# Kernel tuning notes

Hardware: AMD Instinct MI355X
Metric: run time of the kernel (lower is better)

## Reference

```python
import jax, jax.numpy as jnp
import numpy as np

BS, T, N = 16, 50, 100
OBS, ACT, HID, LAT = 40, 8, 64, 16
NEG = -9e15


def _gat(x, adj, w, a_src, a_dst, b, concat, alpha=0.2):
    # x: [B, n, fin]; w: [H, fin, fout]
    h = jnp.einsum('bni,hio->bhno', x, w)
    e_src = jnp.einsum('bhno,ho->bhn', h, a_src[..., 0])
    e_dst = jnp.einsum('bhno,ho->bhn', h, a_dst[..., 0])
    e = e_src[:, :, :, None] + e_dst[:, :, None, :]        # [B,H,n,n]
    e = jnp.where(e > 0, e, alpha * e)                     # LeakyReLU
    e = jnp.where(adj[None, None] > 0, e, NEG)             # mask by adjacency
    att = jax.nn.softmax(e, axis=-1)
    hp = jnp.einsum('bhnm,bhmo->bhno', att, h)
    if concat:
        B, H, n, fo = hp.shape
        return jax.nn.elu(hp.transpose(0, 2, 1, 3).reshape(B, n, H * fo) + b)
    return hp.mean(axis=1) + b


def _lstm(x, Wih, Whh, bih, bhh):
    # x: [B, T, H]; PyTorch gate order i, f, g, o
    def step(carry, xt):
        h, c = carry
        g = xt @ Wih + h @ Whh + bih + bhh
        i, f, gg, o = jnp.split(g, 4, axis=-1)
        c = jax.nn.sigmoid(f) * c + jax.nn.sigmoid(i) * jnp.tanh(gg)
        h = jax.nn.sigmoid(o) * jnp.tanh(c)
        return (h, c), h
    h0 = jnp.zeros((x.shape[0], Whh.shape[0]), x.dtype)
    _, ys = jax.lax.scan(step, (h0, h0), x.transpose(1, 0, 2))
    return ys.transpose(1, 0, 2)


def _forward(o, a_prev, m, eps, params, adj):
    (W_obs, b_obs, W_pa, b_pa, W_mk, b_mk, id_emb,
     lWih, lWhh, lbih, lbhh,
     e1w, e1s, e1d, e1b, e2w, e2s, e2d, e2b,
     d1w, d1s, d1d, d1b, d2w, d2s, d2d, d2b,
     d3w, d3s, d3d, d3b) = params
    bs, t, n, _ = o.shape
    # encode: summed embeddings (dropout is identity in eval)
    emb = (o @ W_obs + b_obs) + (a_prev @ W_pa + b_pa) + (m @ W_mk + b_mk) + id_emb[None, None]
    x = emb.transpose(0, 2, 1, 3).reshape(bs * n, t, HID)
    x = _lstm(x, lWih, lWhh, lbih, lbhh)
    x = x.reshape(bs, n, t, HID).transpose(0, 2, 1, 3).reshape(bs * t, n, HID)
    x = _gat(x, adj, e1w, e1s, e1d, e1b, True)
    x = _gat(x, adj, e2w, e2s, e2d, e2b, False)
    logits = x.reshape(bs, t, n, 2 * LAT).mean(axis=-2)    # AverageGlobalPool over nodes
    mu, logvar = jnp.split(logits, 2, axis=-1)
    z = mu + eps * jnp.exp(0.5 * logvar)                   # reparameterize
    zu = jnp.repeat(z[:, :, None, :], n, axis=2)           # RepeatGlobalUnpool
    d = jnp.concatenate([emb, zu], axis=-1).reshape(bs * t, n, HID + LAT)
    d = _gat(d, adj, d1w, d1s, d1d, d1b, True)
    d = _gat(d, adj, d2w, d2s, d2d, d2b, True)
    d = _gat(d, adj, d3w, d3s, d3d, d3b, False)
    a_recon = d.reshape(bs, t, n, ACT) * m
    return a_recon, mu, logvar


def setup_inputs() -> dict:
    key = jax.random.key(0)
    it = iter(jax.random.split(key, 48))
    def nrm(shape, s=0.1):
        return s * jax.random.normal(next(it), shape, jnp.float32)
    inp = {}
    inp['o'] = jax.random.normal(next(it), (BS, T, N, OBS), jnp.float32)
    inp['a_prev'] = jax.random.uniform(next(it), (BS, T, N, ACT), jnp.float32)
    inp['m'] = (jax.random.uniform(next(it), (BS, T, N, ACT)) > 0.5).astype(jnp.float32)
    inp['eps'] = jax.random.normal(next(it), (BS, T, LAT), jnp.float32)
    adj = jax.random.randint(next(it), (N, N), 0, 2).astype(jnp.int32)
    inp['adj'] = adj.at[jnp.arange(N), jnp.arange(N)].set(1)
    inp['W_obs'] = nrm((OBS, HID)); inp['b_obs'] = jnp.zeros((HID,), jnp.float32)
    inp['W_pa'] = nrm((ACT, HID)); inp['b_pa'] = jnp.zeros((HID,), jnp.float32)
    inp['W_mk'] = nrm((ACT, HID)); inp['b_mk'] = jnp.zeros((HID,), jnp.float32)
    inp['id_emb'] = nrm((N, HID), 1.0)
    inp['lWih'] = nrm((HID, 4 * HID)); inp['lWhh'] = nrm((HID, 4 * HID))
    inp['lbih'] = jnp.zeros((4 * HID,), jnp.float32); inp['lbhh'] = jnp.zeros((4 * HID,), jnp.float32)
    def gat_p(pfx, H, fin, fout, bdim):
        inp[pfx + 'w'] = nrm((H, fin, fout))
        inp[pfx + 's'] = nrm((H, fout, 1))
        inp[pfx + 'd'] = nrm((H, fout, 1))
        inp[pfx + 'b'] = jnp.zeros((bdim,), jnp.float32)
    gat_p('e1', 4, HID, HID // 4, HID)
    gat_p('e2', 1, HID, 2 * LAT, 2 * LAT)
    gat_p('d1', 4, LAT + HID, HID // 4, HID)
    gat_p('d2', 4, HID, HID // 4, HID)
    gat_p('d3', 1, HID, ACT, ACT)
    return inp


def reference(o, a_prev, m, eps, adj, W_obs, b_obs, W_pa, b_pa, W_mk, b_mk, id_emb,
              lWih, lWhh, lbih, lbhh,
              e1w, e1s, e1d, e1b, e2w, e2s, e2d, e2b,
              d1w, d1s, d1d, d1b, d2w, d2s, d2d, d2b,
              d3w, d3s, d3d, d3b):
    params = (W_obs, b_obs, W_pa, b_pa, W_mk, b_mk, id_emb,
              lWih, lWhh, lbih, lbhh,
              e1w, e1s, e1d, e1b, e2w, e2s, e2d, e2b,
              d1w, d1s, d1d, d1b, d2w, d2s, d2d, d2b,
              d3w, d3s, d3d, d3b)
    return _forward(o, a_prev, m, eps, params, adj)
```

## Files before the change

kernel.cpp:

```cpp
#include <hip/hip_runtime.h>

#define BS  16
#define TT  50
#define NN  100
#define OBSF 40
#define ACTF 8
#define HIDF 64
#define LATF 16

typedef __attribute__((ext_vector_type(8))) short bf16x8;
typedef __attribute__((ext_vector_type(4))) float f32x4;

__device__ __forceinline__ float sigmf(float x) { return 1.f / (1.f + __expf(-x)); }
__device__ __forceinline__ float tanh_fast(float x) { return 1.f - 2.f / (__expf(2.f * x) + 1.f); }
__device__ __forceinline__ short bf16s_rne(float a) {
    unsigned u = __float_as_uint(a); u += 0x7fffu + ((u >> 16) & 1u);
    return (short)(u >> 16);
}
__device__ __forceinline__ unsigned bf16pk_rne(float a, float b) {
    unsigned ua = __float_as_uint(a); ua += 0x7fffu + ((ua >> 16) & 1u);
    unsigned ub = __float_as_uint(b); ub += 0x7fffu + ((ub >> 16) & 1u);
    return (ua >> 16) | (ub & 0xffff0000u);
}

__global__ void adjmask_kernel(const int* __restrict__ adj, unsigned long long* __restrict__ mask) {
    int n = threadIdx.x;
    if (n < NN) {
        unsigned long long w0 = 0ull, w1 = 0ull;
        for (int m = 0; m < 64; ++m)  if (adj[n * NN + m] > 0) w0 |= (1ull << m);
        for (int m = 64; m < NN; ++m) if (adj[n * NN + m] > 0) w1 |= (1ull << (m - 64));
        mask[2 * n] = w0; mask[2 * n + 1] = w1;
    }
}

__global__ void emb_kernel(const float* __restrict__ o, const float* __restrict__ ap,
                           const float* __restrict__ mk,
                           const float* __restrict__ Wobs, const float* __restrict__ bobs,
                           const float* __restrict__ Wpa, const float* __restrict__ bpa,
                           const float* __restrict__ Wmk, const float* __restrict__ bmk,
                           const float* __restrict__ idemb, float* __restrict__ emb) {
    int g = blockIdx.x;
    int n = g % NN;
    int j = threadIdx.x;
    __shared__ float so[OBSF], sa[ACTF], sm[ACTF];
    if (j < OBSF) so[j] = o[(size_t)g * OBSF + j];
    if (j >= 40 && j < 48) sa[j - 40] = ap[(size_t)g * ACTF + (j - 40)];
    if (j >= 48 && j < 56) sm[j - 48] = mk[(size_t)g * ACTF + (j - 48)];
    __syncthreads();
    float acc = bobs[j] + bpa[j] + bmk[j] + idemb[n * HIDF + j];
    #pragma unroll
    for (int k = 0; k < OBSF; ++k) acc += so[k] * Wobs[k * HIDF + j];
    #pragma unroll
    for (int k = 0; k < ACTF; ++k) acc += sa[k] * Wpa[k * HIDF + j] + sm[k] * Wmk[k * HIDF + j];
    emb[(size_t)g * HIDF + j] = acc;
}

__launch_bounds__(256)
__global__ void lstm_mfma_kernel(const float* __restrict__ emb,
                                 const float* __restrict__ Wih, const float* __restrict__ Whh,
                                 const float* __restrict__ bih, const float* __restrict__ bhh,
                                 float* __restrict__ xenc) {
    constexpr int GSTRIDE = 260;
    __shared__ __align__(16) float gbuf[16 * GSTRIDE];
    __shared__ __align__(16) short embt[2][16 * 72];
    __shared__ __align__(16) short hbuf[16 * 72];

    const int tid = threadIdx.x;
    const int wv = tid >> 6, lane = tid & 63, q = lane >> 4, c = lane & 15;

    const int seq = tid >> 4;
    const int part = tid & 15;
    const int s = blockIdx.x * 16 + seq;
    const int b = s / NN, n = s % NN;
    const size_t ebase = ((size_t)b * (TT * NN) + n) * HIDF + part * 4;
    const int u0 = part * 4;
    const size_t xbase = ((size_t)b * (TT * NN) + n) * HIDF + u0;

    union { short s8[8]; bf16x8 v; } bf[2][2][4];
    {
        const int colb = wv * 64 + c;
        #pragma unroll
        for (int m = 0; m < 2; ++m) {
            const float* W = m ? Whh : Wih;
            #pragma unroll
            for (int kc = 0; kc < 2; ++kc)
                #pragma unroll
                for (int nt = 0; nt < 4; ++nt)
                    #pragma unroll
                    for (int j = 0; j < 8; ++j)
                        bf[m][kc][nt].s8[j] = bf16s_rne(W[(size_t)(kc * 32 + q * 8 + j) * 256 + colb + nt * 16]);
        }
    }
    float4 bi, bfo, bg, bo;
    {
        float* bp[4] = {&bi.x, &bfo.x, &bg.x, &bo.x};
        #pragma unroll
        for (int gsel = 0; gsel < 4; ++gsel)
            #pragma unroll
            for (int r = 0; r < 4; ++r)
                bp[gsel][r] = bih[gsel * 64 + u0 + r] + bhh[gsel * 64 + u0 + r];
    }
    for (int i = tid; i < 16 * 72 / 2; i += 256) ((unsigned*)hbuf)[i] = 0u;
    {
        float4 e0 = *(const float4*)&emb[ebase];
        uint2 pk; pk.x = bf16pk_rne(e0.x, e0.y); pk.y = bf16pk_rne(e0.z, e0.w);
        *(uint2*)&embt[0][seq * 72 + part * 4] = pk;
    }
    float cst[4] = {0.f, 0.f, 0.f, 0.f};
    __syncthreads();

    for (int t = 0; t < TT; ++t) {
        float4 pre;
        if (t + 1 < TT) pre = *(const float4*)&emb[ebase + (size_t)(t + 1) * (NN * HIDF)];
        const short* et = &embt[t & 1][0];
        bf16x8 a_e0 = *(const bf16x8*)&et[c * 72 + q * 8];
        bf16x8 a_e1 = *(const bf16x8*)&et[c * 72 + 32 + q * 8];
        bf16x8 a_h0 = *(const bf16x8*)&hbuf[c * 72 + q * 8];
        bf16x8 a_h1 = *(const bf16x8*)&hbuf[c * 72 + 32 + q * 8];
        f32x4 acc[4];
        #pragma unroll
        for (int nt = 0; nt < 4; ++nt) {
            f32x4 a = {0.f, 0.f, 0.f, 0.f};
            a = __builtin_amdgcn_mfma_f32_16x16x32_bf16(a_e0, bf[0][0][nt].v, a, 0, 0, 0);
            a = __builtin_amdgcn_mfma_f32_16x16x32_bf16(a_e1, bf[0][1][nt].v, a, 0, 0, 0);
            a = __builtin_amdgcn_mfma_f32_16x16x32_bf16(a_h0, bf[1][0][nt].v, a, 0, 0, 0);
            a = __builtin_amdgcn_mfma_f32_16x16x32_bf16(a_h1, bf[1][1][nt].v, a, 0, 0, 0);
            acc[nt] = a;
        }
        #pragma unroll
        for (int nt = 0; nt < 4; ++nt)
            #pragma unroll
            for (int r = 0; r < 4; ++r)
                gbuf[(q * 4 + r) * GSTRIDE + wv * 64 + nt * 16 + c] = acc[nt][r];
        __syncthreads();
        if (t + 1 < TT) {
            uint2 pk; pk.x = bf16pk_rne(pre.x, pre.y); pk.y = bf16pk_rne(pre.z, pre.w);
            *(uint2*)&embt[(t + 1) & 1][seq * 72 + part * 4] = pk;
        }
        float4 gi = *(const float4*)&gbuf[seq * GSTRIDE + u0];
        float4 gf = *(const float4*)&gbuf[seq * GSTRIDE + 64 + u0];
        float4 gg = *(const float4*)&gbuf[seq * GSTRIDE + 128 + u0];
        float4 go = *(const float4*)&gbuf[seq * GSTRIDE + 192 + u0];
        float hv[4];
        {
            float gir[4] = {gi.x + bi.x, gi.y + bi.y, gi.z + bi.z, gi.w + bi.w};
            float gfr[4] = {gf.x + bfo.x, gf.y + bfo.y, gf.z + bfo.z, gf.w + bfo.w};
            float ggr[4] = {gg.x + bg.x, gg.y + bg.y, gg.z + bg.z, gg.w + bg.w};
            float gor[4] = {go.x + bo.x, go.y + bo.y, go.z + bo.z, go.w + bo.w};
            #pragma unroll
            for (int r = 0; r < 4; ++r) {
                cst[r] = sigmf(gfr[r]) * cst[r] + sigmf(gir[r]) * tanh_fast(ggr[r]);
                hv[r] = sigmf(gor[r]) * tanh_fast(cst[r]);
            }
        }
        uint2 hpk; hpk.x = bf16pk_rne(hv[0], hv[1]); hpk.y = bf16pk_rne(hv[2], hv[3]);
        *(uint2*)&hbuf[seq * 72 + u0] = hpk;
        float4 xo; xo.x = hv[0]; xo.y = hv[1]; xo.z = hv[2]; xo.w = hv[3];
        *(float4*)&xenc[xbase + (size_t)t * (NN * HIDF)] = xo;
        __syncthreads();
    }
}

template <int FIN1, int FIN2, int H, int FOUT, int SPLIT, int OUTMODE>
__launch_bounds__(256)
__global__ void gat_kernel(const float* __restrict__ x1, const float* __restrict__ x2,
                           const float* __restrict__ w, const float* __restrict__ asrc,
                           const float* __restrict__ adst, const float* __restrict__ bias,
                           const unsigned long long* __restrict__ adjmask,
                           const float* __restrict__ mgate, float* __restrict__ out) {
    constexpr int FIN = FIN1 + FIN2;
    constexpr int HF = H * FOUT;
    constexpr int NPT = 256 / HF;
    constexpr int ROWS = (NN + NPT - 1) / NPT;
    constexpr int SB = NN * (FIN > HF ? FIN : HF);
    __shared__ __align__(16) float sbuf[SB];
    __shared__ __align__(16) float ses[H * NN];
    __shared__ __align__(16) float sed[H * NN];
    __shared__ unsigned long long smask[2 * NN];
    int g = blockIdx.x;
    int tid = threadIdx.x;

    for (int i = tid; i < NN * FIN1; i += 256) {
        int n = i / FIN1, k = i % FIN1;
        sbuf[n * FIN + k] = x1[((size_t)g * NN + n) * FIN1 + k];
    }
    if constexpr (FIN2 > 0) {
        for (int i = tid; i < NN * FIN2; i += 256) {
            int n = i / FIN2, k = i % FIN2;
            sbuf[n * FIN + FIN1 + k] = x2[(size_t)g * FIN2 + k];
        }
    }
    if (tid < 2 * NN) smask[tid] = adjmask[tid];
    __syncthreads();

    const int ho = tid % HF;
    const int h = ho / FOUT, o = ho % FOUT;
    const int n0 = tid / HF;
    float racc[ROWS];
    {
        float wcol[FIN];
        #pragma unroll
        for (int k = 0; k < FIN; ++k) wcol[k] = w[(h * FIN + k) * FOUT + o];
        const float as = asrc[ho], ad = adst[ho];
        #pragma unroll
        for (int r = 0; r < ROWS; ++r) {
            int n = n0 + r * NPT;
            float acc = 0.f;
            if (ROWS * NPT == NN || n < NN) {
                const float4* row = (const float4*)&sbuf[n * FIN];
                #pragma unroll
                for (int k4 = 0; k4 < FIN / 4; ++k4) {
                    float4 xv = row[k4];
                    acc += xv.x * wcol[4 * k4] + xv.y * wcol[4 * k4 + 1]
                         + xv.z * wcol[4 * k4 + 2] + xv.w * wcol[4 * k4 + 3];
                }
            }
            racc[r] = acc;
            float vs = acc * as, vd = acc * ad;
            #pragma unroll
            for (int off = FOUT / 2; off >= 1; off >>= 1) {
                vs += __shfl_xor(vs, off, 64);
                vd += __shfl_xor(vd, off, 64);
            }
            if (o == 0 && (ROWS * NPT == NN || n < NN)) {
                ses[h * NN + n] = vs; sed[h * NN + n] = vd;
            }
        }
    }
    __syncthreads();
    #pragma unroll
    for (int r = 0; r < ROWS; ++r) {
        int n = n0 + r * NPT;
        if (ROWS * NPT == NN || n < NN) sbuf[n * HF + ho] = racc[r];
    }
    __syncthreads();

    constexpr int FT = FOUT / SPLIT;
    constexpr int ITEMS = H * NN * SPLIT;
    for (int idx = tid; idx < ITEMS; idx += 256) {
        int h2 = idx / (NN * SPLIT);
        int rem = idx % (NN * SPLIT);
        int n = rem / SPLIT;
        int os = (rem % SPLIT) * FT;
        unsigned long long m0 = smask[2 * n], m1 = smask[2 * n + 1];
        float esn = ses[h2 * NN + n];
        float denom = 0.f;
        float acc[FT];
        #pragma unroll
        for (int qq = 0; qq < FT; ++qq) acc[qq] = 0.f;
        const float4* sed4 = (const float4*)&sed[h2 * NN];
        #pragma unroll 2
        for (int g4 = 0; g4 < NN / 4; ++g4) {
            float4 ev = sed4[g4];
            unsigned int bits = (g4 < 16) ? (unsigned int)(m0 >> (4 * g4))
                                          : (unsigned int)(m1 >> (4 * g4 - 64));
            float e0 = esn + ev.x; e0 = (e0 > 0.f) ? e0 : 0.2f * e0;
            float e1 = esn + ev.y; e1 = (e1 > 0.f) ? e1 : 0.2f * e1;
            float e2 = esn + ev.z; e2 = (e2 > 0.f) ? e2 : 0.2f * e2;
            float e3 = esn + ev.w; e3 = (e3 > 0.f) ? e3 : 0.2f * e3;
            float p0 = (bits & 1u) ? __expf(e0) : 0.f;
            float p1 = (bits & 2u) ? __expf(e1) : 0.f;
            float p2 = (bits & 4u) ? __expf(e2) : 0.f;
            float p3 = (bits & 8u) ? __expf(e3) : 0.f;
            denom += (p0 + p1) + (p2 + p3);
            const float* r0 = &sbuf[(4 * g4 + 0) * HF + h2 * FOUT + os];
            const float* r1 = &sbuf[(4 * g4 + 1) * HF + h2 * FOUT + os];
            const float* r2 = &sbuf[(4 * g4 + 2) * HF + h2 * FOUT + os];
            const float* r3 = &sbuf[(4 * g4 + 3) * HF + h2 * FOUT + os];
            #pragma unroll
            for (int q4 = 0; q4 < FT / 4; ++q4) {
                float4 v0 = ((const float4*)r0)[q4];
                float4 v1 = ((const float4*)r1)[q4];
                float4 v2 = ((const float4*)r2)[q4];
                float4 v3 = ((const float4*)r3)[q4];
                acc[4 * q4 + 0] += p0 * v0.x + p1 * v1.x + p2 * v2.x + p3 * v3.x;
                acc[4 * q4 + 1] += p0 * v0.y + p1 * v1.y + p2 * v2.y + p3 * v3.y;
                acc[4 * q4 + 2] += p0 * v0.z + p1 * v1.z + p2 * v2.z + p3 * v3.z;
                acc[4 * q4 + 3] += p0 * v0.w + p1 * v1.w + p2 * v2.w + p3 * v3.w;
            }
        }
        float inv = 1.f / denom;
        if constexpr (OUTMODE == 0) {
            float4* op = (float4*)&out[((size_t)g * NN + n) * HF + h2 * FOUT + os];
            #pragma unroll
            for (int q4 = 0; q4 < FT / 4; ++q4) {
                float4 v;
                float a0 = acc[4 * q4 + 0] * inv + bias[h2 * FOUT + os + 4 * q4 + 0];
                float a1 = acc[4 * q4 + 1] * inv + bias[h2 * FOUT + os + 4 * q4 + 1];
                float a2 = acc[4 * q4 + 2] * inv + bias[h2 * FOUT + os + 4 * q4 + 2];
                float a3 = acc[4 * q4 + 3] * inv + bias[h2 * FOUT + os + 4 * q4 + 3];
                v.x = (a0 > 0.f) ? a0 : (__expf(a0) - 1.f);
                v.y = (a1 > 0.f) ? a1 : (__expf(a1) - 1.f);
                v.z = (a2 > 0.f) ? a2 : (__expf(a2) - 1.f);
                v.w = (a3 > 0.f) ? a3 : (__expf(a3) - 1.f);
                op[q4] = v;
            }
        } else if constexpr (OUTMODE == 1) {
            float4* op = (float4*)&out[((size_t)g * NN + n) * FOUT + os];
            #pragma unroll
            for (int q4 = 0; q4 < FT / 4; ++q4) {
                float4 v;
                v.x = acc[4 * q4 + 0] * inv + bias[os + 4 * q4 + 0];
                v.y = acc[4 * q4 + 1] * inv + bias[os + 4 * q4 + 1];
                v.z = acc[4 * q4 + 2] * inv + bias[os + 4 * q4 + 2];
                v.w = acc[4 * q4 + 3] * inv + bias[os + 4 * q4 + 3];
                op[q4] = v;
            }
        } else {
            size_t base = ((size_t)g * NN + n) * FOUT + os;
            float4* op = (float4*)&out[base];
            const float4* mp = (const float4*)&mgate[base];
            #pragma unroll
            for (int q4 = 0; q4 < FT / 4; ++q4) {
                float4 mv = mp[q4];
                float4 v;
                v.x = (acc[4 * q4 + 0] * inv + bias[os + 4 * q4 + 0]) * mv.x;
                v.y = (acc[4 * q4 + 1] * inv + bias[os + 4 * q4 + 1]) * mv.y;
                v.z = (acc[4 * q4 + 2] * inv + bias[os + 4 * q4 + 2]) * mv.z;
                v.w = (acc[4 * q4 + 3] * inv + bias[os + 4 * q4 + 3]) * mv.w;
                op[q4] = v;
            }
        }
    }
}

__global__ void pool_kernel(const float* __restrict__ g2, const float* __restrict__ eps,
                            float* __restrict__ z, float* __restrict__ dout) {
    int g = blockIdx.x;
    int c = threadIdx.x;
    __shared__ float s[2 * LATF];
    if (c < 2 * LATF) {
        float sum = 0.f;
        for (int n = 0; n < NN; ++n) sum += g2[((size_t)g * NN + n) * (2 * LATF) + c];
        s[c] = sum * (1.f / NN);
    }
    __syncthreads();
    if (c < LATF) {
        float mu = s[c], lv = s[LATF + c];
        dout[640000 + (size_t)g * LATF + c] = mu;
        dout[652800 + (size_t)g * LATF + c] = lv;
        z[(size_t)g * LATF + c] = mu + eps[(size_t)g * LATF + c] * __expf(0.5f * lv);
    }
}

extern "C" void kernel_launch(void* const* d_in, const int* in_sizes, int n_in,
                              void* d_out, int out_size, void* d_ws, size_t ws_size,
                              hipStream_t stream) {
    const float* o     = (const float*)d_in[0];
    const float* aprev = (const float*)d_in[1];
    const float* mk    = (const float*)d_in[2];
    const float* eps   = (const float*)d_in[3];
    const int*   adj   = (const int*)d_in[4];
    const float* Wobs  = (const float*)d_in[5];
    const float* bobs  = (const float*)d_in[6];
    const float* Wpa   = (const float*)d_in[7];
    const float* bpa   = (const float*)d_in[8];
    const float* Wmk   = (const float*)d_in[9];
    const float* bmk   = (const float*)d_in[10];
    const float* idemb = (const float*)d_in[11];
    const float* lWih  = (const float*)d_in[12];
    const float* lWhh  = (const float*)d_in[13];
    const float* lbih  = (const float*)d_in[14];
    const float* lbhh  = (const float*)d_in[15];
    const float* e1w = (const float*)d_in[16]; const float* e1s = (const float*)d_in[17];
    const float* e1d = (const float*)d_in[18]; const float* e1b = (const float*)d_in[19];
    const float* e2w = (const float*)d_in[20]; const float* e2s = (const float*)d_in[21];
    const float* e2d = (const float*)d_in[22]; const float* e2b = (const float*)d_in[23];
    const float* d1w = (const float*)d_in[24]; const float* d1s = (const float*)d_in[25];
    const float* d1d = (const float*)d_in[26]; const float* d1b = (const float*)d_in[27];
    const float* d2w = (const float*)d_in[28]; const float* d2s = (const float*)d_in[29];
    const float* d2d = (const float*)d_in[30]; const float* d2b = (const float*)d_in[31];
    const float* d3w = (const float*)d_in[32]; const float* d3s = (const float*)d_in[33];
    const float* d3d = (const float*)d_in[34]; const float* d3b = (const float*)d_in[35];

    float* ws   = (float*)d_ws;
    float* emb  = ws;
    float* xenc = ws + 5120000;
    float* g1o  = ws + 10240000;
    float* g2o  = ws + 15360000;
    float* z    = ws + 17920000;
    float* d1o  = ws + 18000000;
    float* d2o  = ws + 23200000;
    unsigned long long* amask = (unsigned long long*)(ws + 30720000);
    float* out = (float*)d_out;

    adjmask_kernel<<<1, 128, 0, stream>>>(adj, amask);
    emb_kernel<<<BS * TT * NN, 64, 0, stream>>>(o, aprev, mk, Wobs, bobs, Wpa, bpa,
                                                Wmk, bmk, idemb, emb);
    lstm_mfma_kernel<<<100, 256, 0, stream>>>(emb, lWih, lWhh, lbih, lbhh, xenc);
    gat_kernel<64, 0, 4, 16, 1, 0><<<800, 256, 0, stream>>>(xenc, nullptr, e1w, e1s, e1d, e1b,
                                                            amask, nullptr, g1o);
    gat_kernel<64, 0, 1, 32, 4, 1><<<800, 256, 0, stream>>>(g1o, nullptr, e2w, e2s, e2d, e2b,
                                                            amask, nullptr, g2o);
    pool_kernel<<<800, 64, 0, stream>>>(g2o, eps, z, out);
    gat_kernel<64, 16, 4, 16, 1, 0><<<800, 256, 0, stream>>>(emb, z, d1w, d1s, d1d, d1b,
                                                             amask, nullptr, d1o);
    gat_kernel<64, 0, 4, 16, 1, 0><<<800, 256, 0, stream>>>(d1o, nullptr, d2w, d2s, d2d, d2b,
                                                            amask, nullptr, d2o);
    gat_kernel<64, 0, 1, 8, 2, 2><<<800, 256, 0, stream>>>(d2o, nullptr, d3w, d3s, d3d, d3b,
                                                           amask, mk, out);
}
```

Before: 514.7 us.

## Store GAT features as fp16 transposed and aggregate with packed fdot2

The GAT kernel now stores the projected node features in shared memory as fp16, transposed to feature-major with rows padded to 112, and does the attention-weighted sum with v_dot2 fp16 dot products over 8 neighbours per step. The broadcast second input (the latent z) is no longer copied into every row; its contribution is folded in once per thread as a dot product. This is meant to cut shared-memory footprint and traffic and the FMA count in the aggregation loop. In exchange, attention weights and features are rounded to fp16 (round toward zero), which lowers accuracy and risks overflow when exp values grow large.

```diff
diff --git a/kernel.cpp b/kernel.cpp
--- a/kernel.cpp
+++ b/kernel.cpp
@@ -10,6 +10,7 @@
 
 typedef __attribute__((ext_vector_type(8))) short bf16x8;
 typedef __attribute__((ext_vector_type(4))) float f32x4;
+typedef __fp16 f16x2 __attribute__((ext_vector_type(2)));
 
 __device__ __forceinline__ float sigmf(float x) { return 1.f / (1.f + __expf(-x)); }
 __device__ __forceinline__ float tanh_fast(float x) { return 1.f - 2.f / (__expf(2.f * x) + 1.f); }
@@ -172,23 +173,25 @@
     constexpr int HF = H * FOUT;
     constexpr int NPT = 256 / HF;
     constexpr int ROWS = (NN + NPT - 1) / NPT;
-    constexpr int SB = NN * (FIN > HF ? FIN : HF);
-    __shared__ __align__(16) float sbuf[SB];
-    __shared__ __align__(16) float ses[H * NN];
-    __shared__ __align__(16) float sed[H * NN];
+    constexpr int SXB = NN * FIN1 * 4;
+    constexpr int SHB = HF * 112 * 2;
+    constexpr int R1 = (SXB > SHB) ? SXB : SHB;
+    __shared__ __align__(16) char smem[R1];
+    float* sx = (float*)smem;
+    __fp16* sh16 = (__fp16*)smem;
+    __shared__ float sz[FIN2 > 0 ? FIN2 : 1];
+    __shared__ __align__(16) float ses[H * 112];
+    __shared__ __align__(16) float sed[H * 112];
     __shared__ unsigned long long smask[2 * NN];
     int g = blockIdx.x;
     int tid = threadIdx.x;
 
     for (int i = tid; i < NN * FIN1; i += 256) {
         int n = i / FIN1, k = i % FIN1;
-        sbuf[n * FIN + k] = x1[((size_t)g * NN + n) * FIN1 + k];
+        sx[n * FIN1 + k] = x1[((size_t)g * NN + n) * FIN1 + k];
     }
     if constexpr (FIN2 > 0) {
-        for (int i = tid; i < NN * FIN2; i += 256) {
-            int n = i / FIN2, k = i % FIN2;
-            sbuf[n * FIN + FIN1 + k] = x2[(size_t)g * FIN2 + k];
-        }
+        if (tid < FIN2) sz[tid] = x2[(size_t)g * FIN2 + tid];
     }
     if (tid < 2 * NN) smask[tid] = adjmask[tid];
     __syncthreads();
@@ -200,16 +203,21 @@
     {
         float wcol[FIN];
         #pragma unroll
-        for (int k = 0; k < FIN; ++k) wcol[k] = w[(h * FIN + k) * FOUT + o];
+        for (int k = 0; k < FIN; ++k) wcol[k] = w[((size_t)h * FIN + k) * FOUT + o];
+        float zdot = 0.f;
+        if constexpr (FIN2 > 0) {
+            #pragma unroll
+            for (int k = 0; k < FIN2; ++k) zdot += sz[k] * wcol[FIN1 + k];
+        }
         const float as = asrc[ho], ad = adst[ho];
         #pragma unroll
         for (int r = 0; r < ROWS; ++r) {
             int n = n0 + r * NPT;
-            float acc = 0.f;
+            float acc = zdot;
             if (ROWS * NPT == NN || n < NN) {
-                const float4* row = (const float4*)&sbuf[n * FIN];
+                const float4* row = (const float4*)&sx[n * FIN1];
                 #pragma unroll
-                for (int k4 = 0; k4 < FIN / 4; ++k4) {
+                for (int k4 = 0; k4 < FIN1 / 4; ++k4) {
                     float4 xv = row[k4];
                     acc += xv.x * wcol[4 * k4] + xv.y * wcol[4 * k4 + 1]
                          + xv.z * wcol[4 * k4 + 2] + xv.w * wcol[4 * k4 + 3];
@@ -223,7 +231,7 @@
                 vd += __shfl_xor(vd, off, 64);
             }
             if (o == 0 && (ROWS * NPT == NN || n < NN)) {
-                ses[h * NN + n] = vs; sed[h * NN + n] = vd;
+                ses[h * 112 + n] = vs; sed[h * 112 + n] = vd;
             }
         }
     }
@@ -231,8 +239,12 @@
     #pragma unroll
     for (int r = 0; r < ROWS; ++r) {
         int n = n0 + r * NPT;
-        if (ROWS * NPT == NN || n < NN) sbuf[n * HF + ho] = racc[r];
-    }
+        if (ROWS * NPT == NN || n < NN) sh16[ho * 112 + n] = (__fp16)racc[r];
+    }
+    for (int i = tid; i < HF * 12; i += 256)
+        sh16[(i / 12) * 112 + 100 + (i % 12)] = (__fp16)0.f;
+    for (int i = tid; i < H * 12; i += 256)
+        sed[(i / 12) * 112 + 100 + (i % 12)] = 0.f;
     __syncthreads();
 
     constexpr int FT = FOUT / SPLIT;
@@ -243,40 +255,49 @@
         int n = rem / SPLIT;
         int os = (rem % SPLIT) * FT;
         unsigned long long m0 = smask[2 * n], m1 = smask[2 * n + 1];
-        float esn = ses[h2 * NN + n];
+        float esn = ses[h2 * 112 + n];
         float denom = 0.f;
         float acc[FT];
         #pragma unroll
         for (int qq = 0; qq < FT; ++qq) acc[qq] = 0.f;
-        const float4* sed4 = (const float4*)&sed[h2 * NN];
+        const float4* sedf4 = (const float4*)&sed[h2 * 112];
+        const __fp16* hb = &sh16[(h2 * FOUT + os) * 112];
         #pragma unroll 2
-        for (int g4 = 0; g4 < NN / 4; ++g4) {
-            float4 ev = sed4[g4];
-            unsigned int bits = (g4 < 16) ? (unsigned int)(m0 >> (4 * g4))
-                                          : (unsigned int)(m1 >> (4 * g4 - 64));
-            float e0 = esn + ev.x; e0 = (e0 > 0.f) ? e0 : 0.2f * e0;
-            float e1 = esn + ev.y; e1 = (e1 > 0.f) ? e1 : 0.2f * e1;
-            float e2 = esn + ev.z; e2 = (e2 > 0.f) ? e2 : 0.2f * e2;
-            float e3 = esn + ev.w; e3 = (e3 > 0.f) ? e3 : 0.2f * e3;
-            float p0 = (bits & 1u) ? __expf(e0) : 0.f;
-            float p1 = (bits & 2u) ? __expf(e1) : 0.f;
-            float p2 = (bits & 4u) ? __expf(e2) : 0.f;
-            float p3 = (bits & 8u) ? __expf(e3) : 0.f;
-            denom += (p0 + p1) + (p2 + p3);
-            const float* r0 = &sbuf[(4 * g4 + 0) * HF + h2 * FOUT + os];
-            const float* r1 = &sbuf[(4 * g4 + 1) * HF + h2 * FOUT + os];
-            const float* r2 = &sbuf[(4 * g4 + 2) * HF + h2 * FOUT + os];
-            const float* r3 = &sbuf[(4 * g4 + 3) * HF + h2 * FOUT + os];
-            #pragma unroll
-            for (int q4 = 0; q4 < FT / 4; ++q4) {
-                float4 v0 = ((const float4*)r0)[q4];
-                float4 v1 = ((const float4*)r1)[q4];
-                float4 v2 = ((const float4*)r2)[q4];
-                float4 v3 = ((const float4*)r3)[q4];
-                acc[4 * q4 + 0] += p0 * v0.x + p1 * v1.x + p2 * v2.x + p3 * v3.x;
-                acc[4 * q4 + 1] += p0 * v0.y + p1 * v1.y + p2 * v2.y + p3 * v3.y;
-                acc[4 * q4 + 2] += p0 * v0.z + p1 * v1.z + p2 * v2.z + p3 * v3.z;
-                acc[4 * q4 + 3] += p0 * v0.w + p1 * v1.w + p2 * v2.w + p3 * v3.w;
+        for (int gg = 0; gg < 13; ++gg) {
+            unsigned mb = (gg < 8) ? (unsigned)(m0 >> (8 * gg)) & 0xffu
+                                   : (unsigned)(m1 >> (8 * (gg - 8))) & 0xffu;
+            float4 edA = sedf4[2 * gg];
+            float4 edB = sedf4[2 * gg + 1];
+            float e0 = esn + edA.x; e0 = fmaxf(e0, 0.2f * e0);
+            float e1 = esn + edA.y; e1 = fmaxf(e1, 0.2f * e1);
+            float e2 = esn + edA.z; e2 = fmaxf(e2, 0.2f * e2);
+            float e3 = esn + edA.w; e3 = fmaxf(e3, 0.2f * e3);
+            float e4 = esn + edB.x; e4 = fmaxf(e4, 0.2f * e4);
+            float e5 = esn + edB.y; e5 = fmaxf(e5, 0.2f * e5);
+            float e6 = esn + edB.z; e6 = fmaxf(e6, 0.2f * e6);
+            float e7 = esn + edB.w; e7 = fmaxf(e7, 0.2f * e7);
+            float p0 = (mb & 1u)   ? __expf(e0) : 0.f;
+            float p1 = (mb & 2u)   ? __expf(e1) : 0.f;
+            float p2 = (mb & 4u)   ? __expf(e2) : 0.f;
+            float p3 = (mb & 8u)   ? __expf(e3) : 0.f;
+            float p4 = (mb & 16u)  ? __expf(e4) : 0.f;
+            float p5 = (mb & 32u)  ? __expf(e5) : 0.f;
+            float p6 = (mb & 64u)  ? __expf(e6) : 0.f;
+            float p7 = (mb & 128u) ? __expf(e7) : 0.f;
+            denom += ((p0 + p1) + (p2 + p3)) + ((p4 + p5) + (p6 + p7));
+            f16x2 q01 = __builtin_amdgcn_cvt_pkrtz(p0, p1);
+            f16x2 q23 = __builtin_amdgcn_cvt_pkrtz(p2, p3);
+            f16x2 q45 = __builtin_amdgcn_cvt_pkrtz(p4, p5);
+            f16x2 q67 = __builtin_amdgcn_cvt_pkrtz(p6, p7);
+            #pragma unroll
+            for (int oo = 0; oo < FT; ++oo) {
+                const f16x2* hp = (const f16x2*)&hb[oo * 112 + gg * 8];
+                float a = acc[oo];
+                a = __builtin_amdgcn_fdot2(q01, hp[0], a, false);
+                a = __builtin_amdgcn_fdot2(q23, hp[1], a, false);
+                a = __builtin_amdgcn_fdot2(q45, hp[2], a, false);
+                a = __builtin_amdgcn_fdot2(q67, hp[3], a, false);
+                acc[oo] = a;
             }
         }
         float inv = 1.f / denom;
```

After: 526.3 us. 1.02x slower.
